# Kernel optimization log

Measured on AMD Instinct MI355X. Metric: run time of the kernel, lower is better.

The kernel has to match this reference:

```python
import jax, jax.numpy as jnp
import numpy as np

B, C, H, W = 8, 64, 128, 128


def setup_inputs() -> dict:
    key = jax.random.key(0)
    k1, k2, k3 = jax.random.split(key, 3)
    x = jax.random.normal(k1, (B, C, H, W), dtype=jnp.float32)
    # offset conv weights: (2C, C, 3, 3), small init like the module (std=0.01)
    W_off = jax.random.normal(k2, (2 * C, C, 3, 3), dtype=jnp.float32) * 0.01
    # following regular conv: (C_out, C, 3, 3)
    W_conv = jax.random.normal(k3, (C, C, 3, 3), dtype=jnp.float32) * 0.05
    b_conv = jnp.zeros((C,), dtype=jnp.float32)
    return {"x": x, "W_off": W_off, "W_conv": W_conv, "b_conv": b_conv}


def _conv2d_same(x, w):
    return jax.lax.conv_general_dilated(
        x, w, window_strides=(1, 1), padding=[(1, 1), (1, 1)],
        dimension_numbers=("NCHW", "OIHW", "NCHW"))


def _deform_offset(x, W_off):
    """Faithful ConvOffset2D: offset conv + clamped 4-corner bilinear gather."""
    b, c, h, w = x.shape
    offsets_ = _conv2d_same(x, W_off)                    # (b, 2c, h, w)
    # torch contiguous view (b,2c,h,w) -> (b*c, h*w, 2): adjacent w elements
    # become the 2 offset components; jnp.reshape matches this exactly.
    offsets = offsets_.reshape(b * c, h * w, 2)
    xf = x.reshape(b * c, h, w)

    gy, gx = jnp.meshgrid(jnp.arange(h), jnp.arange(w), indexing="ij")
    grid = jnp.stack([gy, gx], axis=-1).reshape(-1, 2).astype(x.dtype)  # (h*w, 2)
    coords = offsets + grid[None]                        # (b*c, h*w, 2)

    cy = jnp.clip(coords[..., 0], 0.0, h - 1)
    cx = jnp.clip(coords[..., 1], 0.0, w - 1)
    y0 = jnp.floor(cy)
    y1 = jnp.ceil(cy)
    x0 = jnp.floor(cx)
    x1 = jnp.ceil(cx)

    flat = xf.reshape(-1)                                # (b*c*h*w,)
    base = (jnp.arange(b * c, dtype=jnp.int32) * (h * w))[:, None]

    def gather(yy, xx):
        idx = base + yy.astype(jnp.int32) * w + xx.astype(jnp.int32)
        return flat[idx]

    v_lt = gather(y0, x0)   # (floor y, floor x)
    v_rb = gather(y1, x1)   # (ceil y,  ceil x)
    v_lb = gather(y0, x1)   # (floor y, ceil x)
    v_rt = gather(y1, x0)   # (ceil y,  floor x)

    dy = cy - y0
    dx = cx - x0
    v_t = dy * (v_rt - v_lt) + v_lt
    v_b = dy * (v_rb - v_lb) + v_lb
    out = dx * (v_b - v_t) + v_t                         # (b*c, h*w)
    return out.reshape(b, c, h, w)


def reference(x, W_off, W_conv, b_conv):
    x_def = _deform_offset(x, W_off)
    out = _conv2d_same(x_def, W_conv) + b_conv[None, :, None, None]
    return out
```

## Files before the change

### kernel.cpp

```cpp
#include <hip/hip_runtime.h>

#define DH 128
#define DW 128
#define DB 8
#define DC 64
constexpr int HW = DH * DW;

typedef __attribute__((ext_vector_type(4))) float f32x4;
typedef __attribute__((ext_vector_type(8))) short bf16x8;
typedef __attribute__((ext_vector_type(4))) unsigned int u32x4;

__device__ __forceinline__ unsigned short f2b(float f) {
    unsigned int u = __builtin_bit_cast(unsigned int, f);
    u = (u + 0x7FFFu + ((u >> 16) & 1u)) >> 16;
    return (unsigned short)u;
}
__device__ __forceinline__ float b2f(unsigned short h) {
    unsigned int u = ((unsigned int)h) << 16;
    return __builtin_bit_cast(float, u);
}

__global__ __launch_bounds__(256) void xpose_kernel(
    const float* __restrict__ x, unsigned short* __restrict__ xh)
{
    __shared__ unsigned short sm[64 * 80];
    const int b = blockIdx.y;
    const int p0 = blockIdx.x * 64;
    const int t = threadIdx.x;
    const int ci = t >> 2, q = t & 3;
    const float* xr = x + ((size_t)b * 64 + ci) * HW + p0;
#pragma unroll
    for (int j = 0; j < 4; ++j) {
        int pix = (j * 4 + q) * 4;
        float4 v = *(const float4*)(xr + pix);
        sm[(pix + 0) * 80 + ci] = f2b(v.x);
        sm[(pix + 1) * 80 + ci] = f2b(v.y);
        sm[(pix + 2) * 80 + ci] = f2b(v.z);
        sm[(pix + 3) * 80 + ci] = f2b(v.w);
    }
    __syncthreads();
    unsigned short* outp = xh + ((size_t)b * HW + p0) * 64;
    for (int i = t; i < 512; i += 256) {
        int pix = i >> 3, cq = i & 7;
        u32x4 v = *(const u32x4*)(sm + pix * 80 + cq * 8);
        *(u32x4*)(outp + pix * 64 + cq * 8) = v;
    }
}

__global__ __launch_bounds__(256) void wprep_kernel(
    const float* __restrict__ w, unsigned short* __restrict__ wt, int cout)
{
    int id = blockIdx.x * 256 + threadIdx.x;
    int total = cout * 64 * 9;
    if (id >= total) return;
    int t = id / (cout * 64);
    int rem = id - t * cout * 64;
    int co = rem >> 6, ci = rem & 63;
    wt[id] = f2b(w[((co * 64) + ci) * 9 + t]);
}

template<int COUT, int M_PER_WAVE, bool HWC_BF16_OUT>
__global__ __launch_bounds__(256) void conv_mfma_kernel(
    const unsigned short* __restrict__ xh,
    const unsigned short* __restrict__ wt,
    const float* __restrict__ bias,
    void* __restrict__ outp)
{
    __shared__ char sm[12800];
    const int tid = threadIdx.x;
    const int b = blockIdx.y;
    const int tile = blockIdx.x;
    const int ty0 = (tile >> 4) * 8, tx0 = (tile & 15) * 8;
    const unsigned short* xb = xh + (size_t)b * HW * 64;

    for (int i = tid; i < 800; i += 256) {
        int hp = i >> 3, cq = i & 7;
        int hy = hp / 10, hx = hp - hy * 10;
        int gy = ty0 + hy - 1, gx = tx0 + hx - 1;
        u32x4 v = {0u, 0u, 0u, 0u};
        if ((unsigned)gy < 128u && (unsigned)gx < 128u)
            v = *(const u32x4*)(xb + (size_t)((gy << 7) + gx) * 64 + cq * 8);
        int byte = (hp * 128 + cq * 16) ^ ((hp & 7) << 4);
        *(u32x4*)(sm + byte) = v;
    }
    __syncthreads();

    const int lane = tid & 63;
    const int wv = tid >> 6;
    const int n = lane & 15;
    const int kg = lane >> 4;
    const int cobase = wv * (M_PER_WAVE * 16);

    int base_hp[4];
#pragma unroll
    for (int nt = 0; nt < 4; ++nt) {
        int tp = nt * 16 + n;
        base_hp[nt] = (tp >> 3) * 10 + (tp & 7);
    }

    f32x4 acc[M_PER_WAVE][4];
#pragma unroll
    for (int mi = 0; mi < M_PER_WAVE; ++mi)
#pragma unroll
        for (int ni = 0; ni < 4; ++ni) acc[mi][ni] = (f32x4){0.f, 0.f, 0.f, 0.f};

#pragma unroll
    for (int ty = 0; ty < 3; ++ty)
#pragma unroll
    for (int tx = 0; tx < 3; ++tx) {
        const int t9 = ty * 3 + tx;
        const int toff = ty * 10 + tx;
#pragma unroll
        for (int kk = 0; kk < 2; ++kk) {
            const int ci0 = kk * 32 + kg * 8;
            bf16x8 a[M_PER_WAVE];
#pragma unroll
            for (int mi = 0; mi < M_PER_WAVE; ++mi)
                a[mi] = *(const bf16x8*)(wt + (size_t)(t9 * COUT + cobase + mi * 16 + n) * 64 + ci0);
#pragma unroll
            for (int ni = 0; ni < 4; ++ni) {
                int hp = base_hp[ni] + toff;
                int byte = (hp * 128 + ci0 * 2) ^ ((hp & 7) << 4);
                bf16x8 bv = *(const bf16x8*)(sm + byte);
#pragma unroll
                for (int mi = 0; mi < M_PER_WAVE; ++mi)
                    acc[mi][ni] = __builtin_amdgcn_mfma_f32_16x16x32_bf16(
                        a[mi], bv, acc[mi][ni], 0, 0, 0);
            }
        }
    }

#pragma unroll
    for (int ni = 0; ni < 4; ++ni) {
        int tp = ni * 16 + n;
        int gp = (ty0 + (tp >> 3)) * 128 + tx0 + (tp & 7);
        if (HWC_BF16_OUT) {
            unsigned short* o = (unsigned short*)outp + ((size_t)b * HW + gp) * COUT;
#pragma unroll
            for (int mi = 0; mi < M_PER_WAVE; ++mi) {
                int co = cobase + mi * 16 + kg * 4;
                uint2 pk;
                pk.x = (unsigned)f2b(acc[mi][ni][0]) | ((unsigned)f2b(acc[mi][ni][1]) << 16);
                pk.y = (unsigned)f2b(acc[mi][ni][2]) | ((unsigned)f2b(acc[mi][ni][3]) << 16);
                *(uint2*)(o + co) = pk;
            }
        } else {
            float* o = (float*)outp + (size_t)b * COUT * HW + gp;
#pragma unroll
            for (int mi = 0; mi < M_PER_WAVE; ++mi) {
                int co = cobase + mi * 16 + kg * 4;
#pragma unroll
                for (int r = 0; r < 4; ++r)
                    o[(size_t)(co + r) * HW] = acc[mi][ni][r] + bias[co + r];
            }
        }
    }
}

__global__ __launch_bounds__(256) void deform_kernel(
    const unsigned short* __restrict__ xh,
    const unsigned short* __restrict__ offs,
    unsigned short* __restrict__ xdef)
{
    int idx = blockIdx.x * 256 + threadIdx.x;
    int ci = idx & 63;
    int bp = idx >> 6;
    int p = bp & (HW - 1);
    int b = bp >> 14;
    int ch = 2 * ci + (p >> 13);
    int pp = (2 * p) & (HW - 1);
    const unsigned short* ob = offs + (size_t)b * HW * 128;
    float oy = b2f(ob[(size_t)pp * 128 + ch]);
    float ox = b2f(ob[(size_t)(pp + 1) * 128 + ch]);
    int gy = p >> 7, gx = p & 127;
    float cy = fminf(fmaxf(oy + (float)gy, 0.f), 127.f);
    float cx = fminf(fmaxf(ox + (float)gx, 0.f), 127.f);
    float y0f = floorf(cy), x0f = floorf(cx);
    int y0 = (int)y0f, x0i = (int)x0f;
    int y1 = (int)ceilf(cy), x1 = (int)ceilf(cx);
    const unsigned short* pl = xh + (size_t)b * HW * 64 + ci;
    float v_lt = b2f(pl[(size_t)(y0 * 128 + x0i) * 64]);
    float v_rb = b2f(pl[(size_t)(y1 * 128 + x1) * 64]);
    float v_lb = b2f(pl[(size_t)(y0 * 128 + x1) * 64]);
    float v_rt = b2f(pl[(size_t)(y1 * 128 + x0i) * 64]);
    float dy = cy - y0f, dx = cx - x0f;
    float v_t = fmaf(dy, v_rt - v_lt, v_lt);
    float v_b = fmaf(dy, v_rb - v_lb, v_lb);
    xdef[(size_t)bp * 64 + ci] = f2b(fmaf(dx, v_b - v_t, v_t));
}

extern "C" void kernel_launch(void* const* d_in, const int* in_sizes, int n_in,
                              void* d_out, int out_size, void* d_ws, size_t ws_size,
                              hipStream_t stream) {
    const float* x      = (const float*)d_in[0];
    const float* W_off  = (const float*)d_in[1];
    const float* W_conv = (const float*)d_in[2];
    const float* b_conv = (const float*)d_in[3];

    unsigned short* xh   = (unsigned short*)d_ws;
    unsigned short* offs = xh + (size_t)DB * HW * 64;
    unsigned short* xdef = offs + (size_t)DB * HW * 128;
    unsigned short* wt1  = xdef + (size_t)DB * HW * 64;
    unsigned short* wt2  = wt1 + 9 * 128 * 64;
    float* out = (float*)d_out;

    xpose_kernel<<<dim3(HW / 64, DB), 256, 0, stream>>>(x, xh);
    wprep_kernel<<<(9 * 128 * 64 + 255) / 256, 256, 0, stream>>>(W_off, wt1, 128);
    wprep_kernel<<<(9 * 64 * 64 + 255) / 256, 256, 0, stream>>>(W_conv, wt2, 64);

    conv_mfma_kernel<128, 2, true><<<dim3(256, DB), 256, 0, stream>>>(
        xh, wt1, nullptr, offs);

    deform_kernel<<<(DB * HW * 64) / 256, 256, 0, stream>>>(xh, offs, xdef);

    conv_mfma_kernel<64, 1, false><<<dim3(256, DB), 256, 0, stream>>>(
        xdef, wt2, b_conv, out);
}
```

Measured before the change: 194.7 us.

## Enlarge conv tiles to 16x16, stage weights in LDS, use 32x32 MFMA

The conv kernel now processes 16x16 pixel tiles with 512 threads. Per-tap weight slices are staged in a double-buffered, swizzled LDS buffer, and the next tap is prefetched through registers while the current one computes. It switches to the 32x32x16 bf16 MFMA with 16-element accumulators, and the two weight-prep launches are merged into one. The goal is to cut redundant global weight loads and halo overhead and to improve MFMA efficiency, at the cost of more LDS, a barrier per tap, and fewer blocks.

```diff
diff --git a/kernel.cpp b/kernel.cpp
--- a/kernel.cpp
+++ b/kernel.cpp
@@ -7,6 +7,7 @@
 constexpr int HW = DH * DW;
 
 typedef __attribute__((ext_vector_type(4))) float f32x4;
+typedef __attribute__((ext_vector_type(16))) float f32x16;
 typedef __attribute__((ext_vector_type(8))) short bf16x8;
 typedef __attribute__((ext_vector_type(4))) unsigned int u32x4;
 
@@ -48,110 +49,167 @@
 }
 
 __global__ __launch_bounds__(256) void wprep_kernel(
-    const float* __restrict__ w, unsigned short* __restrict__ wt, int cout)
+    const float* __restrict__ wo, const float* __restrict__ wc,
+    unsigned short* __restrict__ wt1, unsigned short* __restrict__ wt2)
 {
     int id = blockIdx.x * 256 + threadIdx.x;
-    int total = cout * 64 * 9;
-    if (id >= total) return;
-    int t = id / (cout * 64);
-    int rem = id - t * cout * 64;
-    int co = rem >> 6, ci = rem & 63;
-    wt[id] = f2b(w[((co * 64) + ci) * 9 + t]);
-}
-
-template<int COUT, int M_PER_WAVE, bool HWC_BF16_OUT>
-__global__ __launch_bounds__(256) void conv_mfma_kernel(
+    const int N1 = 9 * 128 * 64, N2 = 9 * 64 * 64;
+    if (id < N1) {
+        int t = id / (128 * 64);
+        int rem = id - t * 128 * 64;
+        int co = rem >> 6, ci = rem & 63;
+        wt1[id] = f2b(wo[(co * 64 + ci) * 9 + t]);
+    } else if (id < N1 + N2) {
+        int k = id - N1;
+        int t = k / (64 * 64);
+        int rem = k - t * 64 * 64;
+        int co = rem >> 6, ci = rem & 63;
+        wt2[k] = f2b(wc[(co * 64 + ci) * 9 + t]);
+    }
+}
+
+template<int COUT, int MI, bool HWC_BF16_OUT>
+__global__ __launch_bounds__(512, 4) void conv_mfma_kernel(
     const unsigned short* __restrict__ xh,
     const unsigned short* __restrict__ wt,
     const float* __restrict__ bias,
     void* __restrict__ outp)
 {
-    __shared__ char sm[12800];
+    constexpr int WBYTES = COUT * 64 * 2;
+    constexpr int SPASS = WBYTES / 8192;
+    __shared__ char sm[41472 + 2 * WBYTES];
+    char* const wbuf0 = sm + 41472;
+    char* const wbuf1 = sm + 41472 + WBYTES;
+
     const int tid = threadIdx.x;
     const int b = blockIdx.y;
-    const int tile = blockIdx.x;
-    const int ty0 = (tile >> 4) * 8, tx0 = (tile & 15) * 8;
+    const int ty0 = (blockIdx.x >> 3) << 4;
+    const int tx0 = (blockIdx.x & 7) << 4;
     const unsigned short* xb = xh + (size_t)b * HW * 64;
 
-    for (int i = tid; i < 800; i += 256) {
+    u32x4 wreg[SPASS];
+    {
+        const char* wsrc = (const char*)wt;
+#pragma unroll
+        for (int s = 0; s < SPASS; ++s) {
+            int L = (s * 512 + tid) * 16;
+            wreg[s] = *(const u32x4*)(wsrc + (L ^ (((L >> 7) & 7) << 4)));
+        }
+    }
+    for (int i = tid; i < 2592; i += 512) {
         int hp = i >> 3, cq = i & 7;
-        int hy = hp / 10, hx = hp - hy * 10;
+        int hy = hp / 18, hx = hp - hy * 18;
         int gy = ty0 + hy - 1, gx = tx0 + hx - 1;
         u32x4 v = {0u, 0u, 0u, 0u};
         if ((unsigned)gy < 128u && (unsigned)gx < 128u)
             v = *(const u32x4*)(xb + (size_t)((gy << 7) + gx) * 64 + cq * 8);
-        int byte = (hp * 128 + cq * 16) ^ ((hp & 7) << 4);
-        *(u32x4*)(sm + byte) = v;
+        *(u32x4*)(sm + ((hp * 128 + cq * 16) ^ ((hp & 7) << 4))) = v;
+    }
+#pragma unroll
+    for (int s = 0; s < SPASS; ++s) {
+        int L = (s * 512 + tid) * 16;
+        *(u32x4*)(wbuf0 + L) = wreg[s];
     }
     __syncthreads();
 
     const int lane = tid & 63;
     const int wv = tid >> 6;
-    const int n = lane & 15;
-    const int kg = lane >> 4;
-    const int cobase = wv * (M_PER_WAVE * 16);
-
-    int base_hp[4];
-#pragma unroll
-    for (int nt = 0; nt < 4; ++nt) {
-        int tp = nt * 16 + n;
-        base_hp[nt] = (tp >> 3) * 10 + (tp & 7);
-    }
-
-    f32x4 acc[M_PER_WAVE][4];
-#pragma unroll
-    for (int mi = 0; mi < M_PER_WAVE; ++mi)
-#pragma unroll
-        for (int ni = 0; ni < 4; ++ni) acc[mi][ni] = (f32x4){0.f, 0.f, 0.f, 0.f};
-
-#pragma unroll
-    for (int ty = 0; ty < 3; ++ty)
-#pragma unroll
-    for (int tx = 0; tx < 3; ++tx) {
-        const int t9 = ty * 3 + tx;
-        const int toff = ty * 10 + tx;
-#pragma unroll
-        for (int kk = 0; kk < 2; ++kk) {
-            const int ci0 = kk * 32 + kg * 8;
-            bf16x8 a[M_PER_WAVE];
-#pragma unroll
-            for (int mi = 0; mi < M_PER_WAVE; ++mi)
-                a[mi] = *(const bf16x8*)(wt + (size_t)(t9 * COUT + cobase + mi * 16 + n) * 64 + ci0);
-#pragma unroll
-            for (int ni = 0; ni < 4; ++ni) {
-                int hp = base_hp[ni] + toff;
-                int byte = (hp * 128 + ci0 * 2) ^ ((hp & 7) << 4);
-                bf16x8 bv = *(const bf16x8*)(sm + byte);
-#pragma unroll
-                for (int mi = 0; mi < M_PER_WAVE; ++mi)
-                    acc[mi][ni] = __builtin_amdgcn_mfma_f32_16x16x32_bf16(
-                        a[mi], bv, acc[mi][ni], 0, 0, 0);
-            }
-        }
-    }
-
-#pragma unroll
-    for (int ni = 0; ni < 4; ++ni) {
-        int tp = ni * 16 + n;
-        int gp = (ty0 + (tp >> 3)) * 128 + tx0 + (tp & 7);
+    const int wm = wv & 1;
+    const int wn = wv >> 1;
+    const int n = lane & 31;
+    const int half = lane >> 5;
+    const int px = n & 15;
+    const int pyb = wn * 4 + (n >> 4);
+    const int swzA = (lane & 7) << 4;
+    const int rowA = (wm * (MI * 32) + n) * 128 + half * 16;
+
+    int hp0[2];
+#pragma unroll
+    for (int ni = 0; ni < 2; ++ni)
+        hp0[ni] = (pyb + ni * 2) * 18 + px;
+
+    f32x16 acc[MI][2];
+#pragma unroll
+    for (int mi = 0; mi < MI; ++mi)
+#pragma unroll
+        for (int ni = 0; ni < 2; ++ni)
+#pragma unroll
+            for (int e = 0; e < 16; ++e) acc[mi][ni][e] = 0.f;
+
+#pragma unroll
+    for (int t9 = 0; t9 < 9; ++t9) {
+        const int toff = (t9 / 3) * 18 + (t9 % 3);
+        const char* wb = (t9 & 1) ? wbuf1 : wbuf0;
+        u32x4 wr[SPASS];
+        if (t9 < 8) {
+            const char* wsrc = (const char*)(wt + (size_t)(t9 + 1) * COUT * 64);
+#pragma unroll
+            for (int s = 0; s < SPASS; ++s) {
+                int L = (s * 512 + tid) * 16;
+                wr[s] = *(const u32x4*)(wsrc + (L ^ (((L >> 7) & 7) << 4)));
+            }
+        }
+#pragma unroll
+        for (int kk = 0; kk < 4; ++kk) {
+            const int kcol = kk * 32;
+            bf16x8 a[MI], bv[2];
+#pragma unroll
+            for (int mi = 0; mi < MI; ++mi)
+                a[mi] = *(const bf16x8*)(wb + ((rowA + mi * 4096 + kcol) ^ swzA));
+#pragma unroll
+            for (int ni = 0; ni < 2; ++ni) {
+                int hp = hp0[ni] + toff;
+                bv[ni] = *(const bf16x8*)(sm + ((hp * 128 + kcol + half * 16) ^ ((hp & 7) << 4)));
+            }
+#pragma unroll
+            for (int mi = 0; mi < MI; ++mi)
+#pragma unroll
+                for (int ni = 0; ni < 2; ++ni)
+                    acc[mi][ni] = __builtin_amdgcn_mfma_f32_32x32x16_bf16(
+                        a[mi], bv[ni], acc[mi][ni], 0, 0, 0);
+        }
+        if (t9 < 8) {
+            char* wbn = ((t9 + 1) & 1) ? wbuf1 : wbuf0;
+#pragma unroll
+            for (int s = 0; s < SPASS; ++s) {
+                int L = (s * 512 + tid) * 16;
+                *(u32x4*)(wbn + L) = wr[s];
+            }
+        }
+        __syncthreads();
+    }
+
+#pragma unroll
+    for (int ni = 0; ni < 2; ++ni) {
+        int py = pyb + ni * 2;
+        int gp = (ty0 + py) * 128 + tx0 + px;
         if (HWC_BF16_OUT) {
             unsigned short* o = (unsigned short*)outp + ((size_t)b * HW + gp) * COUT;
 #pragma unroll
-            for (int mi = 0; mi < M_PER_WAVE; ++mi) {
-                int co = cobase + mi * 16 + kg * 4;
-                uint2 pk;
-                pk.x = (unsigned)f2b(acc[mi][ni][0]) | ((unsigned)f2b(acc[mi][ni][1]) << 16);
-                pk.y = (unsigned)f2b(acc[mi][ni][2]) | ((unsigned)f2b(acc[mi][ni][3]) << 16);
-                *(uint2*)(o + co) = pk;
+            for (int mi = 0; mi < MI; ++mi) {
+                int cob = wm * (MI * 32) + mi * 32 + half * 4;
+#pragma unroll
+                for (int g = 0; g < 4; ++g) {
+                    uint2 pk;
+                    pk.x = (unsigned)f2b(acc[mi][ni][g * 4 + 0]) |
+                           ((unsigned)f2b(acc[mi][ni][g * 4 + 1]) << 16);
+                    pk.y = (unsigned)f2b(acc[mi][ni][g * 4 + 2]) |
+                           ((unsigned)f2b(acc[mi][ni][g * 4 + 3]) << 16);
+                    *(uint2*)(o + cob + g * 8) = pk;
+                }
             }
         } else {
             float* o = (float*)outp + (size_t)b * COUT * HW + gp;
 #pragma unroll
-            for (int mi = 0; mi < M_PER_WAVE; ++mi) {
-                int co = cobase + mi * 16 + kg * 4;
-#pragma unroll
-                for (int r = 0; r < 4; ++r)
-                    o[(size_t)(co + r) * HW] = acc[mi][ni][r] + bias[co + r];
+            for (int mi = 0; mi < MI; ++mi) {
+                int cob = wm * (MI * 32) + mi * 32 + half * 4;
+#pragma unroll
+                for (int g = 0; g < 4; ++g)
+#pragma unroll
+                    for (int r = 0; r < 4; ++r) {
+                        int co = cob + g * 8 + r;
+                        o[(size_t)co * HW] = acc[mi][ni][g * 4 + r] + bias[co];
+                    }
             }
         }
     }
@@ -205,14 +263,14 @@
     float* out = (float*)d_out;
 
     xpose_kernel<<<dim3(HW / 64, DB), 256, 0, stream>>>(x, xh);
-    wprep_kernel<<<(9 * 128 * 64 + 255) / 256, 256, 0, stream>>>(W_off, wt1, 128);
-    wprep_kernel<<<(9 * 64 * 64 + 255) / 256, 256, 0, stream>>>(W_conv, wt2, 64);
-
-    conv_mfma_kernel<128, 2, true><<<dim3(256, DB), 256, 0, stream>>>(
+    wprep_kernel<<<(9 * 128 * 64 + 9 * 64 * 64 + 255) / 256, 256, 0, stream>>>(
+        W_off, W_conv, wt1, wt2);
+
+    conv_mfma_kernel<128, 2, true><<<dim3(64, DB), 512, 0, stream>>>(
         xh, wt1, nullptr, offs);
 
     deform_kernel<<<(DB * HW * 64) / 256, 256, 0, stream>>>(xh, offs, xdef);
 
-    conv_mfma_kernel<64, 1, false><<<dim3(256, DB), 256, 0, stream>>>(
+    conv_mfma_kernel<64, 1, false><<<dim3(64, DB), 512, 0, stream>>>(
         xdef, wt2, b_conv, out);
 }
```

Result: faster. 162.2 us (-16.7%).
